# Kernel optimization log

Hardware: AMD Instinct MI355X
Metric: run time of the kernel (lower is better)

## Reference

```python
import jax, jax.numpy as jnp
import numpy as np

HID = 1024; HEADS = 16; HD = 64; INTER = 4096; NLAYERS = 4
PATCH = 16; IMG_SIZE = 1024; MAXSIDE = IMG_SIZE // PATCH
THETA = 10000.0; EPS = 1e-5; SCALE = HD ** -0.5


def setup_inputs() -> dict:
    key = jax.random.key(0)
    ks = jax.random.split(key, 11)
    s = 0.02
    w = lambda k, shape: jax.random.normal(k, shape, jnp.float32) * s
    return {
        "img0": jax.random.normal(ks[0], (3, 512, 512), jnp.float32),
        "img1": jax.random.normal(ks[1], (3, 512, 256), jnp.float32),
        "conv_w": w(ks[2], (HID, 3, PATCH, PATCH)),
        "ln_pre_w": jnp.ones((HID,), jnp.float32),
        "attn_norm_w": jnp.ones((NLAYERS, HID), jnp.float32),
        "q_w": w(ks[3], (NLAYERS, HID, HID)),
        "k_w": w(ks[4], (NLAYERS, HID, HID)),
        "v_w": w(ks[5], (NLAYERS, HID, HID)),
        "o_w": w(ks[6], (NLAYERS, HID, HID)),
        "ffn_norm_w": jnp.ones((NLAYERS, HID), jnp.float32),
        "gate_w": w(ks[7], (NLAYERS, INTER, HID)),
        "up_w": w(ks[8], (NLAYERS, INTER, HID)),
        "down_w": w(ks[9], (NLAYERS, HID, INTER)),
    }


def _rms(x, wt):
    return x * jax.lax.rsqrt(jnp.mean(x * x, axis=-1, keepdims=True) + EPS) * wt


def _rot_half(x):
    return jnp.concatenate([-x[..., HD // 2:], x[..., :HD // 2]], axis=-1)


def reference(img0, img1, conv_w, ln_pre_w, attn_norm_w, q_w, k_w, v_w, o_w,
              ffn_norm_w, gate_w, up_w, down_w):
    dn = ('NCHW', 'OIHW', 'NCHW')
    grids, embeds = [], []
    for img in (img0, img1):
        p = jax.lax.conv_general_dilated(img[None], conv_w, (PATCH, PATCH),
                                         'VALID', dimension_numbers=dn)  # [1,HID,h,w]
        h, wd = p.shape[2], p.shape[3]
        grids.append((h, wd))
        embeds.append(p.reshape(1, HID, h * wd).transpose(0, 2, 1))
    x = jnp.concatenate(embeds, axis=1)  # [1, S, HID]
    S = x.shape[1]
    x = _rms(x, ln_pre_w)

    # meshgrid position ids: h*MAXSIDE + w per image
    pids = jnp.concatenate([
        (jnp.arange(h)[:, None] * MAXSIDE + jnp.arange(wd)[None, :]).reshape(-1)
        for h, wd in grids])
    # Pixtral 2D RoPE frequency table
    freqs = 1.0 / THETA ** (jnp.arange(0, HD, 2, dtype=jnp.float32) / HD)  # [HD/2]
    fh = jnp.outer(jnp.arange(MAXSIDE, dtype=jnp.float32), freqs[::2])   # [64, HD/4]
    fw = jnp.outer(jnp.arange(MAXSIDE, dtype=jnp.float32), freqs[1::2])  # [64, HD/4]
    inv = jnp.concatenate([
        jnp.broadcast_to(fh[:, None, :], (MAXSIDE, MAXSIDE, HD // 4)),
        jnp.broadcast_to(fw[None, :, :], (MAXSIDE, MAXSIDE, HD // 4))],
        axis=-1).reshape(-1, HD // 2)
    inv = jnp.concatenate([inv, inv], axis=-1)  # [MAXSIDE^2, HD]
    emb = inv[pids]                              # [S, HD]
    cos = jnp.cos(emb)[None, None]               # [1,1,S,HD]
    sin = jnp.sin(emb)[None, None]

    # block-diagonal additive mask (images don't attend across each other)
    neg = jnp.finfo(jnp.float32).min
    mask = jnp.full((S, S), neg, jnp.float32)
    off = 0
    for h, wd in grids:
        n = h * wd
        mask = mask.at[off:off + n, off:off + n].set(0.0)
        off += n

    def layer(xc, p):
        an, qw, kw, vw, ow, fn, gw, uw, dw = p
        hn = _rms(xc, an)
        heads = lambda y, wm: jnp.einsum('bsd,ed->bse', y, wm).reshape(
            1, S, HEADS, HD).transpose(0, 2, 1, 3)  # [1,H,S,D]
        q, k, v = heads(hn, qw), heads(hn, kw), heads(hn, vw)
        q = q * cos + _rot_half(q) * sin
        k = k * cos + _rot_half(k) * sin
        scores = jnp.einsum('bhqd,bhkd->bhqk', q, k) * SCALE + mask
        aw = jax.nn.softmax(scores.astype(jnp.float32), axis=-1).astype(xc.dtype)
        o = jnp.einsum('bhqk,bhkd->bhqd', aw, v).transpose(0, 2, 1, 3).reshape(1, S, HID)
        h2 = xc + jnp.einsum('bsd,ed->bse', o, ow)
        m = _rms(h2, fn)
        ff = jnp.einsum(
            'bsi,di->bsd',
            jax.nn.silu(jnp.einsum('bsd,id->bsi', m, gw)) * jnp.einsum('bsd,id->bsi', m, uw),
            dw)
        return h2 + ff, None

    out, _ = jax.lax.scan(layer, x, (attn_norm_w, q_w, k_w, v_w, o_w,
                                     ffn_norm_w, gate_w, up_w, down_w))
    return out
```

## Files before the change

### kernel.cpp

```cpp
#include <hip/hip_runtime.h>
#include <hip/hip_bf16.h>
#include <math.h>

#define S_TOT 1536
#define S0    1024
#define HID   1024
#define HEADS 16
#define HD    64
#define INTER 4096
#define NLAYERS 4
#define KCONV 768
#define EPSV  1e-5f
#define SCALEV 0.125f
#define QKS   2048

typedef __attribute__((ext_vector_type(8))) __bf16 bf16x8;
typedef __attribute__((ext_vector_type(8))) unsigned short u16x8;
typedef __attribute__((ext_vector_type(4))) float f32x4;
typedef __attribute__((address_space(1))) void gvoid;
typedef __attribute__((address_space(3))) void lvoid;

__device__ __forceinline__ ushort f2bf(float f) {
    union { float f; unsigned u; } v; v.f = f;
    unsigned u = v.u;
    return (ushort)((u + 0x7FFFu + ((u >> 16) & 1u)) >> 16);
}
__device__ __forceinline__ float bf2f(ushort b) {
    union { unsigned u; float f; } v; v.u = ((unsigned)b) << 16;
    return v.f;
}

template<int N> __device__ __forceinline__ void wait_vm() {
    if constexpr (N == 0)      asm volatile("s_waitcnt vmcnt(0)" ::: "memory");
    else if constexpr (N == 2) asm volatile("s_waitcnt vmcnt(2)" ::: "memory");
    else if constexpr (N == 4) asm volatile("s_waitcnt vmcnt(4)" ::: "memory");
    else if constexpr (N == 8) asm volatile("s_waitcnt vmcnt(8)" ::: "memory");
    else                       asm volatile("s_waitcnt vmcnt(0)" ::: "memory");
}

__global__ __launch_bounds__(256) void cvt_kernel(
    const float* __restrict__ src, ushort* __restrict__ dst, int n4)
{
    int i = blockIdx.x * 256 + threadIdx.x;
    if (i < n4) {
        float4 v = ((const float4*)src)[i];
        ushort4 o;
        o.x = f2bf(v.x); o.y = f2bf(v.y); o.z = f2bf(v.z); o.w = f2bf(v.w);
        ((ushort4*)dst)[i] = o;
    }
}

__global__ __launch_bounds__(256) void cvt_layer_kernel(
    const float* __restrict__ qw, const float* __restrict__ kw,
    const float* __restrict__ vw, const float* __restrict__ ow,
    const float* __restrict__ gw, const float* __restrict__ uw,
    const float* __restrict__ dw, ushort* __restrict__ dst)
{
    int i = blockIdx.x * 256 + threadIdx.x;
    int e = i << 2;
    const float* src; int off; size_t de;
    if      (e < (1  << 20)) { src = qw; off = e;             de = e; }
    else if (e < (2  << 20)) { src = kw; off = e - (1 << 20); de = e; }
    else if (e < (3  << 20)) { src = vw; off = e - (2 << 20); de = e; }
    else if (e < (4  << 20)) { src = ow; off = e - (3 << 20); de = e; }
    else if (e < (8  << 20)) {
        src = gw; off = e - (4 << 20);
        int chan = off >> 10, col = off & 1023;
        de = (size_t)(4 << 20) + (size_t)(((chan >> 4) << 5) + (chan & 15)) * 1024 + col;
    }
    else if (e < (12 << 20)) {
        src = uw; off = e - (8 << 20);
        int chan = off >> 10, col = off & 1023;
        de = (size_t)(4 << 20) + (size_t)(((chan >> 4) << 5) + 16 + (chan & 15)) * 1024 + col;
    }
    else                     { src = dw; off = e - (12 << 20); de = e; }
    float4 v = *(const float4*)(src + off);
    ushort4 o;
    o.x = f2bf(v.x); o.y = f2bf(v.y); o.z = f2bf(v.z); o.w = f2bf(v.w);
    *(ushort4*)(dst + de) = o;
}

__global__ __launch_bounds__(256) void im2col_kernel(
    const float* __restrict__ img0, const float* __restrict__ img1,
    ushort* __restrict__ P)
{
    int s = blockIdx.x;
    const float* img; int W, ph, pw;
    if (s < S0) { img = img0; W = 512; ph = s >> 5; pw = s & 31; }
    else { int t = s - S0; img = img1; W = 256; ph = t >> 4; pw = t & 15; }
    for (int k = threadIdx.x; k < KCONV; k += 256) {
        int c = k >> 8; int r = k & 255; int y = r >> 4; int x = r & 15;
        P[(size_t)s * KCONV + k] =
            f2bf(img[(size_t)c * 512 * W + (size_t)(ph * 16 + y) * W + (pw * 16 + x)]);
    }
}

#define GEMM2P_CORE(BM_, BN_, NLA_, NLB_)                                        \
    auto stage = [&](int b, int k0) {                                            \
        _Pragma("unroll")                                                        \
        for (int i_ = 0; i_ < NLA_; ++i_) {                                      \
            int idx = t + i_ * 256;                                              \
            int r_ = idx >> 2, c8_ = (idx & 3) << 3;                             \
            __builtin_amdgcn_global_load_lds(                                    \
                (gvoid*)(A + (size_t)(bm + r_) * K + k0 + c8_),                  \
                (lvoid*)(&As[b][idx * 8]), 16, 0, 0);                            \
        }                                                                        \
        _Pragma("unroll")                                                        \
        for (int i_ = 0; i_ < NLB_; ++i_) {                                      \
            int idx = t + i_ * 256;                                              \
            int r_ = idx >> 2, c8_ = (idx & 3) << 3;                             \
            __builtin_amdgcn_global_load_lds(                                    \
                (gvoid*)(B + (size_t)(bn + r_) * K + k0 + c8_),                  \
                (lvoid*)(&Bs[b][idx * 8]), 16, 0, 0);                            \
        }                                                                        \
    };

template<int BM, int BN, bool OUT_BF16>
__global__ __launch_bounds__(256) void gemm2p(
    const ushort* __restrict__ A, const ushort* __restrict__ B,
    void* __restrict__ Cout, int M, int N, int K)
{
    constexpr int WMT = BM / 32, WNT = BN / 32;
    constexpr int NLA = (BM * 32) / (8 * 256);
    constexpr int NLB = (BN * 32) / (8 * 256);
    constexpr int NL  = NLA + NLB;
    __shared__ ushort As[2][BM * 32];
    __shared__ ushort Bs[2][BN * 32];
    const int t = threadIdx.x;
    const int bm = blockIdx.x * BM, bn = blockIdx.y * BN;
    const int wave = t >> 6, lane = t & 63;
    const int wm = (wave & 1) * (BM / 2), wn = (wave >> 1) * (BN / 2);
    const int frow = lane & 15, fq = lane >> 4;
    GEMM2P_CORE(BM, BN, NLA, NLB)

    f32x4 acc[WMT][WNT];
    #pragma unroll
    for (int i = 0; i < WMT; ++i)
        #pragma unroll
        for (int j = 0; j < WNT; ++j) acc[i][j] = (f32x4){0.f, 0.f, 0.f, 0.f};

    stage(0, 0);
    int cur = 0;
    for (int k0 = 0; k0 < K; k0 += 32) {
        const bool more = (k0 + 32) < K;
        if (more) { stage(cur ^ 1, k0 + 32); wait_vm<NL>(); }
        else      { wait_vm<0>(); }
        __builtin_amdgcn_s_barrier();
        __builtin_amdgcn_sched_barrier(0);
        bf16x8 af[WMT], bfr[WNT];
        #pragma unroll
        for (int i = 0; i < WMT; ++i)
            af[i] = *(const bf16x8*)(&As[cur][(wm + 16 * i + frow) * 32 + fq * 8]);
        #pragma unroll
        for (int j = 0; j < WNT; ++j)
            bfr[j] = *(const bf16x8*)(&Bs[cur][(wn + 16 * j + frow) * 32 + fq * 8]);
        asm volatile("s_waitcnt lgkmcnt(0)" ::: "memory");
        __builtin_amdgcn_sched_barrier(0);
        __builtin_amdgcn_s_barrier();
        #pragma unroll
        for (int i = 0; i < WMT; ++i)
            #pragma unroll
            for (int j = 0; j < WNT; ++j)
                acc[i][j] = __builtin_amdgcn_mfma_f32_16x16x32_bf16(
                    af[i], bfr[j], acc[i][j], 0, 0, 0);
        cur ^= 1;
    }
    #pragma unroll
    for (int i = 0; i < WMT; ++i) {
        #pragma unroll
        for (int j = 0; j < WNT; ++j) {
            #pragma unroll
            for (int r = 0; r < 4; ++r) {
                int row = bm + wm + 16 * i + fq * 4 + r;
                int col = bn + wn + 16 * j + frow;
                float vv = acc[i][j][r];
                if (OUT_BF16) ((ushort*)Cout)[(size_t)row * N + col] = f2bf(vv);
                else          ((float*)Cout)[(size_t)row * N + col] = vv;
            }
        }
    }
}

__global__ __launch_bounds__(256) void gemm2p_qkv(
    const ushort* __restrict__ A, const ushort* __restrict__ B,
    ushort* __restrict__ qkb, ushort* __restrict__ vb,
    const float* __restrict__ cs, const float* __restrict__ sn, int K)
{
    constexpr int BM = 128, BN = 128;
    __shared__ ushort As[2][BM * 32];
    __shared__ ushort Bs[2][BN * 32];
    const int t = threadIdx.x;
    const int bm = blockIdx.x * BM, bn = blockIdx.y * BN;
    const int wave = t >> 6, lane = t & 63;
    const int wm = (wave & 1) * 64, wn = (wave >> 1) * 64;
    const int frow = lane & 15, fq = lane >> 4;
    GEMM2P_CORE(BM, BN, 2, 2)

    f32x4 acc[4][4];
    #pragma unroll
    for (int i = 0; i < 4; ++i)
        #pragma unroll
        for (int j = 0; j < 4; ++j) acc[i][j] = (f32x4){0.f, 0.f, 0.f, 0.f};

    stage(0, 0);
    int cur = 0;
    for (int k0 = 0; k0 < K; k0 += 32) {
        const bool more = (k0 + 32) < K;
        if (more) { stage(cur ^ 1, k0 + 32); wait_vm<4>(); }
        else      { wait_vm<0>(); }
        __builtin_amdgcn_s_barrier();
        __builtin_amdgcn_sched_barrier(0);
        bf16x8 af[4], bfr[4];
        #pragma unroll
        for (int i = 0; i < 4; ++i)
            af[i] = *(const bf16x8*)(&As[cur][(wm + 16 * i + frow) * 32 + fq * 8]);
        #pragma unroll
        for (int j = 0; j < 4; ++j)
            bfr[j] = *(const bf16x8*)(&Bs[cur][(wn + 16 * j + frow) * 32 + fq * 8]);
        asm volatile("s_waitcnt lgkmcnt(0)" ::: "memory");
        __builtin_amdgcn_sched_barrier(0);
        __builtin_amdgcn_s_barrier();
        #pragma unroll
        for (int i = 0; i < 4; ++i)
            #pragma unroll
            for (int j = 0; j < 4; ++j)
                acc[i][j] = __builtin_amdgcn_mfma_f32_16x16x32_bf16(
                    af[i], bfr[j], acc[i][j], 0, 0, 0);
        cur ^= 1;
    }
    const int colbase = bn + wn;
    const int part = colbase >> 10;
    if (part < 2) {
        #pragma unroll
        for (int i = 0; i < 4; ++i) {
            #pragma unroll
            for (int r = 0; r < 4; ++r) {
                int row = bm + wm + 16 * i + fq * 4 + r;
                float cv0 = cs[row * 32 + frow],      sv0 = sn[row * 32 + frow];
                float cv1 = cs[row * 32 + 16 + frow], sv1 = sn[row * 32 + 16 + frow];
                float xa0 = acc[i][0][r], xa1 = acc[i][1][r];
                float xb0 = acc[i][2][r], xb1 = acc[i][3][r];
                ushort* dst = qkb + (size_t)row * QKS + (part << 10) + (colbase & 1023) + frow;
                dst[0]  = f2bf(xa0 * cv0 - xb0 * sv0);
                dst[16] = f2bf(xa1 * cv1 - xb1 * sv1);
                dst[32] = f2bf(xb0 * cv0 + xa0 * sv0);
                dst[48] = f2bf(xb1 * cv1 + xa1 * sv1);
            }
        }
    } else {
        #pragma unroll
        for (int i = 0; i < 4; ++i)
            #pragma unroll
            for (int j = 0; j < 4; ++j)
                #pragma unroll
                for (int r = 0; r < 4; ++r) {
                    int row = bm + wm + 16 * i + fq * 4 + r;
                    vb[(size_t)row * 1024 + (colbase & 1023) + 16 * j + frow] =
                        f2bf(acc[i][j][r]);
                }
    }
}

__global__ __launch_bounds__(256) void gemm2p_gu(
    const ushort* __restrict__ A, const ushort* __restrict__ B,
    ushort* __restrict__ gb, int K)
{
    constexpr int BM = 128, BN = 128;
    __shared__ ushort As[2][BM * 32];
    __shared__ ushort Bs[2][BN * 32];
    const int t = threadIdx.x;
    const int bm = blockIdx.x * BM, bn = blockIdx.y * BN;
    const int wave = t >> 6, lane = t & 63;
    const int wm = (wave & 1) * 64, wn = (wave >> 1) * 64;
    const int frow = lane & 15, fq = lane >> 4;
    GEMM2P_CORE(BM, BN, 2, 2)

    f32x4 acc[4][4];
    #pragma unroll
    for (int i = 0; i < 4; ++i)
        #pragma unroll
        for (int j = 0; j < 4; ++j) acc[i][j] = (f32x4){0.f, 0.f, 0.f, 0.f};

    stage(0, 0);
    int cur = 0;
    for (int k0 = 0; k0 < K; k0 += 32) {
        const bool more = (k0 + 32) < K;
        if (more) { stage(cur ^ 1, k0 + 32); wait_vm<4>(); }
        else      { wait_vm<0>(); }
        __builtin_amdgcn_s_barrier();
        __builtin_amdgcn_sched_barrier(0);
        bf16x8 af[4], bfr[4];
        #pragma unroll
        for (int i = 0; i < 4; ++i)
            af[i] = *(const bf16x8*)(&As[cur][(wm + 16 * i + frow) * 32 + fq * 8]);
        #pragma unroll
        for (int j = 0; j < 4; ++j)
            bfr[j] = *(const bf16x8*)(&Bs[cur][(wn + 16 * j + frow) * 32 + fq * 8]);
        asm volatile("s_waitcnt lgkmcnt(0)" ::: "memory");
        __builtin_amdgcn_sched_barrier(0);
        __builtin_amdgcn_s_barrier();
        #pragma unroll
        for (int i = 0; i < 4; ++i)
            #pragma unroll
            for (int j = 0; j < 4; ++j)
                acc[i][j] = __builtin_amdgcn_mfma_f32_16x16x32_bf16(
                    af[i], bfr[j], acc[i][j], 0, 0, 0);
        cur ^= 1;
    }
    #pragma unroll
    for (int i = 0; i < 4; ++i) {
        #pragma unroll
        for (int jp = 0; jp < 2; ++jp) {
            int chan = ((bn + wn) >> 1) + jp * 16 + frow;
            #pragma unroll
            for (int r = 0; r < 4; ++r) {
                int row = bm + wm + 16 * i + fq * 4 + r;
                float g = acc[i][2 * jp][r], u = acc[i][2 * jp + 1][r];
                float sg = 1.f / (1.f + __expf(-g));
                gb[(size_t)row * INTER + chan] = f2bf(g * sg * u);
            }
        }
    }
}

template<int SPLITK>
__global__ __launch_bounds__(256) void gemm2p_sk(
    const ushort* __restrict__ A, const ushort* __restrict__ B,
    float* __restrict__ P, int M, int N, int K)
{
    constexpr int BM = 128, BN = 128;
    __shared__ ushort As[2][BM * 32];
    __shared__ ushort Bs[2][BN * 32];
    const int t = threadIdx.x;
    const int bm = blockIdx.x * BM, bn = blockIdx.y * BN;
    const int kc = K / SPLITK;
    const int kb = blockIdx.z * kc, ke = kb + kc;
    const int wave = t >> 6, lane = t & 63;
    const int wm = (wave & 1) * 64, wn = (wave >> 1) * 64;
    const int frow = lane & 15, fq = lane >> 4;
    GEMM2P_CORE(BM, BN, 2, 2)

    f32x4 acc[4][4];
    #pragma unroll
    for (int i = 0; i < 4; ++i)
        #pragma unroll
        for (int j = 0; j < 4; ++j) acc[i][j] = (f32x4){0.f, 0.f, 0.f, 0.f};

    stage(0, kb);
    int cur = 0;
    for (int k0 = kb; k0 < ke; k0 += 32) {
        const bool more = (k0 + 32) < ke;
        if (more) { stage(cur ^ 1, k0 + 32); wait_vm<4>(); }
        else      { wait_vm<0>(); }
        __builtin_amdgcn_s_barrier();
        __builtin_amdgcn_sched_barrier(0);
        bf16x8 af[4], bfr[4];
        #pragma unroll
        for (int i = 0; i < 4; ++i)
            af[i] = *(const bf16x8*)(&As[cur][(wm + 16 * i + frow) * 32 + fq * 8]);
        #pragma unroll
        for (int j = 0; j < 4; ++j)
            bfr[j] = *(const bf16x8*)(&Bs[cur][(wn + 16 * j + frow) * 32 + fq * 8]);
        asm volatile("s_waitcnt lgkmcnt(0)" ::: "memory");
        __builtin_amdgcn_sched_barrier(0);
        __builtin_amdgcn_s_barrier();
        #pragma unroll
        for (int i = 0; i < 4; ++i)
            #pragma unroll
            for (int j = 0; j < 4; ++j)
                acc[i][j] = __builtin_amdgcn_mfma_f32_16x16x32_bf16(
                    af[i], bfr[j], acc[i][j], 0, 0, 0);
        cur ^= 1;
    }
    float* Pz = P + (size_t)blockIdx.z * M * N;
    #pragma unroll
    for (int i = 0; i < 4; ++i) {
        #pragma unroll
        for (int j = 0; j < 4; ++j) {
            #pragma unroll
            for (int r = 0; r < 4; ++r) {
                int row = bm + wm + 16 * i + fq * 4 + r;
                int col = bn + wn + 16 * j + frow;
                Pz[(size_t)row * N + col] = acc[i][j][r];
            }
        }
    }
}

__global__ __launch_bounds__(256) void reduce4_kernel(
    const float* __restrict__ P, float* __restrict__ x, int n4)
{
    int i = blockIdx.x * 256 + threadIdx.x;
    if (i >= n4) return;
    const int n = n4 << 2;
    float4 a  = ((const float4*)x)[i];
    float4 p0 = ((const float4*)P)[i];
    float4 p1 = ((const float4*)(P + (size_t)n))[i];
    float4 p2 = ((const float4*)(P + (size_t)2 * n))[i];
    float4 p3 = ((const float4*)(P + (size_t)3 * n))[i];
    a.x += p0.x + p1.x + p2.x + p3.x;
    a.y += p0.y + p1.y + p2.y + p3.y;
    a.z += p0.z + p1.z + p2.z + p3.z;
    a.w += p0.w + p1.w + p2.w + p3.w;
    ((float4*)x)[i] = a;
}

__global__ __launch_bounds__(256) void rms_kernel(
    const float* __restrict__ in, const float* __restrict__ w,
    float* __restrict__ out)
{
    int row = blockIdx.x;
    const float* xr = in + (size_t)row * HID;
    float ss = 0.f;
    for (int i = threadIdx.x; i < HID; i += 256) { float v = xr[i]; ss += v * v; }
    #pragma unroll
    for (int off = 32; off > 0; off >>= 1) ss += __shfl_down(ss, off, 64);
    __shared__ float red[4];
    int wid = threadIdx.x >> 6;
    if ((threadIdx.x & 63) == 0) red[wid] = ss;
    __syncthreads();
    if (threadIdx.x == 0)
        red[0] = rsqrtf((red[0] + red[1] + red[2] + red[3]) / HID + EPSV);
    __syncthreads();
    float rs = red[0];
    for (int i = threadIdx.x; i < HID; i += 256)
        out[(size_t)row * HID + i] = xr[i] * rs * w[i];
}

__global__ __launch_bounds__(256) void rms_bf_kernel(
    const float* __restrict__ in, const float* __restrict__ w,
    ushort* __restrict__ out)
{
    int row = blockIdx.x;
    const float* xr = in + (size_t)row * HID;
    float ss = 0.f;
    for (int i = threadIdx.x; i < HID; i += 256) { float v = xr[i]; ss += v * v; }
    #pragma unroll
    for (int off = 32; off > 0; off >>= 1) ss += __shfl_down(ss, off, 64);
    __shared__ float red[4];
    int wid = threadIdx.x >> 6;
    if ((threadIdx.x & 63) == 0) red[wid] = ss;
    __syncthreads();
    if (threadIdx.x == 0)
        red[0] = rsqrtf((red[0] + red[1] + red[2] + red[3]) / HID + EPSV);
    __syncthreads();
    float rs = red[0];
    for (int i = threadIdx.x; i < HID; i += 256)
        out[(size_t)row * HID + i] = f2bf(xr[i] * rs * w[i]);
}

__global__ void rope_tab_kernel(float* __restrict__ cs, float* __restrict__ sn)
{
    int s = blockIdx.x; int j = threadIdx.x;
    int h, w;
    if (s < S0) { h = s >> 5; w = s & 31; }
    else { int t = s - S0; h = t >> 4; w = t & 15; }
    float f;
    if (j < 16) f = (float)h * powf(10000.f, -(4.f * j) / 64.f);
    else        f = (float)w * powf(10000.f, -(4.f * (j - 16) + 2.f) / 64.f);
    cs[s * 32 + j] = cosf(f);
    sn[s * 32 + j] = sinf(f);
}

__global__ __launch_bounds__(256) void vtrans_bf_kernel(
    const ushort* __restrict__ vb, ushort* __restrict__ vT)
{
    __shared__ ushort T[64][72];
    int st = blockIdx.x;
    int hh = blockIdx.y;
    int s0 = st << 6;
    int t = threadIdx.x;
    #pragma unroll
    for (int i = 0; i < 2; ++i) {
        int u = t + (i << 8);
        int r = u >> 3, c8 = (u & 7) << 3;
        u16x8 v = *(const u16x8*)(vb + (size_t)(s0 + r) * 1024 + hh * HD + c8);
        *(u16x8*)(&T[r][c8]) = v;
    }
    __syncthreads();
    int d = t >> 2, sg = (t & 3) << 4;
    ushort buf[16];
    #pragma unroll
    for (int j = 0; j < 16; ++j) buf[j] = T[sg + j][d];
    ushort* dst = vT + ((size_t)hh * HD + d) * S_TOT + s0 + sg;
    *(u16x8*)dst = *(u16x8*)buf;
    *(u16x8*)(dst + 8) = *(u16x8*)(buf + 8);
}

__global__ __launch_bounds__(256) void flash_mfma_kernel(
    const ushort* __restrict__ qkb, const ushort* __restrict__ vT,
    ushort* __restrict__ o)
{
    __shared__ ushort Ks[64 * 72];
    __shared__ ushort Vt[64 * 72];
    __shared__ ushort Ps[4 * 16 * 72];
    int tile = blockIdx.x;
    int hh = blockIdx.y;
    int segStart, q0, nkt;
    if (tile < 16) { segStart = 0; q0 = tile << 6; nkt = 16; }
    else { segStart = S0; q0 = S0 + ((tile - 16) << 6); nkt = 8; }
    const int t = threadIdx.x;
    const int wave = t >> 6, lane = t & 63;
    const int c = lane & 15, fq = lane >> 4;
    const int wq = wave << 4;
    ushort* Pw = Ps + wave * 16 * 72;

    bf16x8 qf[2];
    #pragma unroll
    for (int ks = 0; ks < 2; ++ks)
        qf[ks] = *(const bf16x8*)(qkb + (size_t)(q0 + wq + c) * QKS + hh * HD + ks * 32 + fq * 8);

    float m_i[4], l_i[4];
    f32x4 accO[4];
    #pragma unroll
    for (int r = 0; r < 4; ++r) { m_i[r] = -1e30f; l_i[r] = 0.f; }
    #pragma unroll
    for (int nt = 0; nt < 4; ++nt) accO[nt] = (f32x4){0.f, 0.f, 0.f, 0.f};

    for (int kt = 0; kt < nkt; ++kt) {
        int kbase = segStart + (kt << 6);
        __syncthreads();
        #pragma unroll
        for (int i = 0; i < 2; ++i) {
            int u = t + (i << 8);
            int r = u >> 3, c8 = (u & 7) << 3;
            u16x8 kv = *(const u16x8*)(qkb + (size_t)(kbase + r) * QKS + 1024 + hh * HD + c8);
            *(u16x8*)(Ks + r * 72 + c8) = kv;
            u16x8 vv = *(const u16x8*)(vT + ((size_t)hh * HD + r) * S_TOT + kbase + c8);
            *(u16x8*)(Vt + r * 72 + c8) = vv;
        }
        __syncthreads();

        f32x4 acc[4];
        #pragma unroll
        for (int nt = 0; nt < 4; ++nt) acc[nt] = (f32x4){0.f, 0.f, 0.f, 0.f};
        #pragma unroll
        for (int ks = 0; ks < 2; ++ks) {
            #pragma unroll
            for (int nt = 0; nt < 4; ++nt) {
                bf16x8 bfr = *(const bf16x8*)(Ks + (nt * 16 + c) * 72 + ks * 32 + fq * 8);
                acc[nt] = __builtin_amdgcn_mfma_f32_16x16x32_bf16(qf[ks], bfr, acc[nt], 0, 0, 0);
            }
        }

        #pragma unroll
        for (int r = 0; r < 4; ++r) {
            float s0v = acc[0][r] * SCALEV, s1v = acc[1][r] * SCALEV;
            float s2v = acc[2][r] * SCALEV, s3v = acc[3][r] * SCALEV;
            float rm = fmaxf(fmaxf(s0v, s1v), fmaxf(s2v, s3v));
            #pragma unroll
            for (int msk = 1; msk < 16; msk <<= 1)
                rm = fmaxf(rm, __shfl_xor(rm, msk, 64));
            float mn = fmaxf(m_i[r], rm);
            float al = __expf(m_i[r] - mn);
            float p0 = __expf(s0v - mn), p1 = __expf(s1v - mn);
            float p2 = __expf(s2v - mn), p3 = __expf(s3v - mn);
            float rs = p0 + p1 + p2 + p3;
            #pragma unroll
            for (int msk = 1; msk < 16; msk <<= 1)
                rs += __shfl_xor(rs, msk, 64);
            l_i[r] = l_i[r] * al + rs;
            m_i[r] = mn;
            #pragma unroll
            for (int nt = 0; nt < 4; ++nt) accO[nt][r] *= al;
            int qrow = (fq << 2) + r;
            Pw[qrow * 72 + 0  + c] = f2bf(p0);
            Pw[qrow * 72 + 16 + c] = f2bf(p1);
            Pw[qrow * 72 + 32 + c] = f2bf(p2);
            Pw[qrow * 72 + 48 + c] = f2bf(p3);
        }

        #pragma unroll
        for (int ks = 0; ks < 2; ++ks) {
            bf16x8 pa = *(const bf16x8*)(Pw + c * 72 + ks * 32 + fq * 8);
            #pragma unroll
            for (int nt = 0; nt < 4; ++nt) {
                bf16x8 bv = *(const bf16x8*)(Vt + (nt * 16 + c) * 72 + ks * 32 + fq * 8);
                accO[nt] = __builtin_amdgcn_mfma_f32_16x16x32_bf16(pa, bv, accO[nt], 0, 0, 0);
            }
        }
    }

    #pragma unroll
    for (int r = 0; r < 4; ++r) {
        float inv = 1.f / l_i[r];
        int row = q0 + wq + (fq << 2) + r;
        #pragma unroll
        for (int nt = 0; nt < 4; ++nt)
            o[(size_t)row * HID + hh * HD + nt * 16 + c] = f2bf(accO[nt][r] * inv);
    }
}

__global__ __launch_bounds__(256) void copy_kernel(
    const float* __restrict__ src, float* __restrict__ dst, int n)
{
    int i = blockIdx.x * 256 + threadIdx.x;
    if (i < n) dst[i] = src[i];
}

extern "C" void kernel_launch(void* const* d_in, const int* in_sizes, int n_in,
                              void* d_out, int out_size, void* d_ws, size_t ws_size,
                              hipStream_t stream)
{
    const float* img0        = (const float*)d_in[0];
    const float* img1        = (const float*)d_in[1];
    const float* conv_w      = (const float*)d_in[2];
    const float* ln_pre_w    = (const float*)d_in[3];
    const float* attn_norm_w = (const float*)d_in[4];
    const float* q_w         = (const float*)d_in[5];
    const float* k_w         = (const float*)d_in[6];
    const float* v_w         = (const float*)d_in[7];
    const float* o_w         = (const float*)d_in[8];
    const float* ffn_norm_w  = (const float*)d_in[9];
    const float* gate_w      = (const float*)d_in[10];
    const float* up_w        = (const float*)d_in[11];
    const float* down_w      = (const float*)d_in[12];

    char* p = (char*)d_ws;
    float* x    = (float*)p;   p += (size_t)1572864 * 4;
    float* cs   = (float*)p;   p += (size_t)49152 * 4;
    float* sn   = (float*)p;   p += (size_t)49152 * 4;
    ushort* qkb = (ushort*)p;  p += (size_t)3145728 * 2;
    ushort* vb  = (ushort*)p;  p += (size_t)1572864 * 2;
    ushort* vTb = (ushort*)p;  p += (size_t)1572864 * 2;
    ushort* hnb = (ushort*)p;  p += (size_t)1572864 * 2;
    ushort* obb = (ushort*)p;  p += (size_t)1572864 * 2;
    ushort* gb  = (ushort*)p;  p += (size_t)6291456 * 2;
    float* skP  = (float*)p;   p += (size_t)6291456 * 4;
    ushort* Pb  = (ushort*)p;  p += (size_t)1179648 * 2;
    ushort* cvb = (ushort*)p;  p += (size_t)786432 * 2;
    ushort* wbuf= (ushort*)p;  p += (size_t)16777216 * 2;

    ushort* wqkv = wbuf;
    ushort* wo   = wbuf + 3145728;
    ushort* wgu  = wbuf + 4194304;
    ushort* wdn  = wbuf + 12582912;

    dim3 blk(256);

    cvt_kernel<<<768, blk, 0, stream>>>(conv_w, cvb, 786432 / 4);
    im2col_kernel<<<S_TOT, blk, 0, stream>>>(img0, img1, Pb);
    gemm2p<64, 64, false><<<dim3(24, 16), blk, 0, stream>>>(
        Pb, cvb, x, S_TOT, HID, KCONV);
    rms_kernel<<<S_TOT, blk, 0, stream>>>(x, ln_pre_w, x);
    rope_tab_kernel<<<S_TOT, 32, 0, stream>>>(cs, sn);

    for (int l = 0; l < NLAYERS; ++l) {
        cvt_layer_kernel<<<16384, blk, 0, stream>>>(
            q_w + (size_t)l * 1048576, k_w + (size_t)l * 1048576,
            v_w + (size_t)l * 1048576, o_w + (size_t)l * 1048576,
            gate_w + (size_t)l * 4194304, up_w + (size_t)l * 4194304,
            down_w + (size_t)l * 4194304, wbuf);

        rms_bf_kernel<<<S_TOT, blk, 0, stream>>>(x, attn_norm_w + (size_t)l * HID, hnb);
        gemm2p_qkv<<<dim3(12, 24), blk, 0, stream>>>(
            hnb, wqkv, qkb, vb, cs, sn, HID);
        vtrans_bf_kernel<<<dim3(24, HEADS), blk, 0, stream>>>(vb, vTb);
        flash_mfma_kernel<<<dim3(24, HEADS), blk, 0, stream>>>(qkb, vTb, obb);
        gemm2p_sk<4><<<dim3(12, 8, 4), blk, 0, stream>>>(
            obb, wo, skP, S_TOT, HID, HID);
        reduce4_kernel<<<1536, blk, 0, stream>>>(skP, x, S_TOT * HID / 4);
        rms_bf_kernel<<<S_TOT, blk, 0, stream>>>(x, ffn_norm_w + (size_t)l * HID, hnb);
        gemm2p_gu<<<dim3(12, 64), blk, 0, stream>>>(hnb, wgu, gb, HID);
        gemm2p_sk<4><<<dim3(12, 8, 4), blk, 0, stream>>>(
            gb, wdn, skP, S_TOT, HID, INTER);
        reduce4_kernel<<<1536, blk, 0, stream>>>(skP, x, S_TOT * HID / 4);
    }
    copy_kernel<<<(S_TOT * HID) / 256, blk, 0, stream>>>(x, (float*)d_out, S_TOT * HID);
}
```

Baseline: 927.9 us.

## Triple-buffer GEMM loads, fuse V transpose into QKV epilogue, fuse reduce+RMS

All GEMM kernels move from a double-buffered to a triple-buffered LDS pipeline with a single barrier per k-step, and raise wave priority around the MFMA block. The QKV GEMM epilogue now writes V directly in transposed per-head layout, which removes the separate transpose kernel and its buffer. The split-K reduction after the O projection is fused with the following RMS norm into one kernel, saving a launch and a pass over x. Extra LDS per block may lower occupancy, and the transposed V stores are strided 8-byte writes.

```diff
diff --git a/kernel.cpp b/kernel.cpp
--- a/kernel.cpp
+++ b/kernel.cpp
@@ -95,7 +95,7 @@
     }
 }
 
-#define GEMM2P_CORE(BM_, BN_, NLA_, NLB_)                                        \
+#define STAGE_LAMBDA(NLA_, NLB_)                                                 \
     auto stage = [&](int b, int k0) {                                            \
         _Pragma("unroll")                                                        \
         for (int i_ = 0; i_ < NLA_; ++i_) {                                      \
@@ -115,8 +115,25 @@
         }                                                                        \
     };
 
+#define LOOP3B_HEAD(NL_, KBASE_)                                                 \
+    stage(0, KBASE_); stage(1, KBASE_ + 32);                                     \
+    int cbuf = 0, sbuf = 2;                                                      \
+    for (int kt = 0; kt < NKT; ++kt) {                                           \
+        if (kt + 1 < NKT) wait_vm<NL_>(); else wait_vm<0>();                     \
+        __builtin_amdgcn_sched_barrier(0);                                       \
+        __builtin_amdgcn_s_barrier();                                            \
+        __builtin_amdgcn_sched_barrier(0);                                       \
+        if (kt + 2 < NKT) {                                                      \
+            stage(sbuf, KBASE_ + ((kt + 2) << 5));                               \
+            sbuf = (sbuf == 2) ? 0 : sbuf + 1;                                   \
+        }
+
+#define LOOP3B_TAIL                                                              \
+        cbuf = (cbuf == 2) ? 0 : cbuf + 1;                                       \
+    }
+
 template<int BM, int BN, bool OUT_BF16>
-__global__ __launch_bounds__(256) void gemm2p(
+__global__ __launch_bounds__(256) void gemm3b(
     const ushort* __restrict__ A, const ushort* __restrict__ B,
     void* __restrict__ Cout, int M, int N, int K)
 {
@@ -124,14 +141,14 @@
     constexpr int NLA = (BM * 32) / (8 * 256);
     constexpr int NLB = (BN * 32) / (8 * 256);
     constexpr int NL  = NLA + NLB;
-    __shared__ ushort As[2][BM * 32];
-    __shared__ ushort Bs[2][BN * 32];
+    __shared__ ushort As[3][BM * 32];
+    __shared__ ushort Bs[3][BN * 32];
     const int t = threadIdx.x;
     const int bm = blockIdx.x * BM, bn = blockIdx.y * BN;
     const int wave = t >> 6, lane = t & 63;
     const int wm = (wave & 1) * (BM / 2), wn = (wave >> 1) * (BN / 2);
     const int frow = lane & 15, fq = lane >> 4;
-    GEMM2P_CORE(BM, BN, NLA, NLB)
+    STAGE_LAMBDA(NLA, NLB)
 
     f32x4 acc[WMT][WNT];
     #pragma unroll
@@ -139,32 +156,24 @@
         #pragma unroll
         for (int j = 0; j < WNT; ++j) acc[i][j] = (f32x4){0.f, 0.f, 0.f, 0.f};
 
-    stage(0, 0);
-    int cur = 0;
-    for (int k0 = 0; k0 < K; k0 += 32) {
-        const bool more = (k0 + 32) < K;
-        if (more) { stage(cur ^ 1, k0 + 32); wait_vm<NL>(); }
-        else      { wait_vm<0>(); }
-        __builtin_amdgcn_s_barrier();
-        __builtin_amdgcn_sched_barrier(0);
+    const int NKT = K >> 5;
+    LOOP3B_HEAD(NL, 0)
         bf16x8 af[WMT], bfr[WNT];
         #pragma unroll
         for (int i = 0; i < WMT; ++i)
-            af[i] = *(const bf16x8*)(&As[cur][(wm + 16 * i + frow) * 32 + fq * 8]);
+            af[i] = *(const bf16x8*)(&As[cbuf][(wm + 16 * i + frow) * 32 + fq * 8]);
         #pragma unroll
         for (int j = 0; j < WNT; ++j)
-            bfr[j] = *(const bf16x8*)(&Bs[cur][(wn + 16 * j + frow) * 32 + fq * 8]);
-        asm volatile("s_waitcnt lgkmcnt(0)" ::: "memory");
-        __builtin_amdgcn_sched_barrier(0);
-        __builtin_amdgcn_s_barrier();
+            bfr[j] = *(const bf16x8*)(&Bs[cbuf][(wn + 16 * j + frow) * 32 + fq * 8]);
+        __builtin_amdgcn_s_setprio(1);
         #pragma unroll
         for (int i = 0; i < WMT; ++i)
             #pragma unroll
             for (int j = 0; j < WNT; ++j)
                 acc[i][j] = __builtin_amdgcn_mfma_f32_16x16x32_bf16(
                     af[i], bfr[j], acc[i][j], 0, 0, 0);
-        cur ^= 1;
-    }
+        __builtin_amdgcn_s_setprio(0);
+    LOOP3B_TAIL
     #pragma unroll
     for (int i = 0; i < WMT; ++i) {
         #pragma unroll
@@ -181,20 +190,20 @@
     }
 }
 
-__global__ __launch_bounds__(256) void gemm2p_qkv(
+__global__ __launch_bounds__(256) void gemm3b_qkv(
     const ushort* __restrict__ A, const ushort* __restrict__ B,
-    ushort* __restrict__ qkb, ushort* __restrict__ vb,
+    ushort* __restrict__ qkb, ushort* __restrict__ vT,
     const float* __restrict__ cs, const float* __restrict__ sn, int K)
 {
     constexpr int BM = 128, BN = 128;
-    __shared__ ushort As[2][BM * 32];
-    __shared__ ushort Bs[2][BN * 32];
+    __shared__ ushort As[3][BM * 32];
+    __shared__ ushort Bs[3][BN * 32];
     const int t = threadIdx.x;
     const int bm = blockIdx.x * BM, bn = blockIdx.y * BN;
     const int wave = t >> 6, lane = t & 63;
     const int wm = (wave & 1) * 64, wn = (wave >> 1) * 64;
     const int frow = lane & 15, fq = lane >> 4;
-    GEMM2P_CORE(BM, BN, 2, 2)
+    STAGE_LAMBDA(2, 2)
 
     f32x4 acc[4][4];
     #pragma unroll
@@ -202,32 +211,24 @@
         #pragma unroll
         for (int j = 0; j < 4; ++j) acc[i][j] = (f32x4){0.f, 0.f, 0.f, 0.f};
 
-    stage(0, 0);
-    int cur = 0;
-    for (int k0 = 0; k0 < K; k0 += 32) {
-        const bool more = (k0 + 32) < K;
-        if (more) { stage(cur ^ 1, k0 + 32); wait_vm<4>(); }
-        else      { wait_vm<0>(); }
-        __builtin_amdgcn_s_barrier();
-        __builtin_amdgcn_sched_barrier(0);
+    const int NKT = K >> 5;
+    LOOP3B_HEAD(4, 0)
         bf16x8 af[4], bfr[4];
         #pragma unroll
         for (int i = 0; i < 4; ++i)
-            af[i] = *(const bf16x8*)(&As[cur][(wm + 16 * i + frow) * 32 + fq * 8]);
+            af[i] = *(const bf16x8*)(&As[cbuf][(wm + 16 * i + frow) * 32 + fq * 8]);
         #pragma unroll
         for (int j = 0; j < 4; ++j)
-            bfr[j] = *(const bf16x8*)(&Bs[cur][(wn + 16 * j + frow) * 32 + fq * 8]);
-        asm volatile("s_waitcnt lgkmcnt(0)" ::: "memory");
-        __builtin_amdgcn_sched_barrier(0);
-        __builtin_amdgcn_s_barrier();
+            bfr[j] = *(const bf16x8*)(&Bs[cbuf][(wn + 16 * j + frow) * 32 + fq * 8]);
+        __builtin_amdgcn_s_setprio(1);
         #pragma unroll
         for (int i = 0; i < 4; ++i)
             #pragma unroll
             for (int j = 0; j < 4; ++j)
                 acc[i][j] = __builtin_amdgcn_mfma_f32_16x16x32_bf16(
                     af[i], bfr[j], acc[i][j], 0, 0, 0);
-        cur ^= 1;
-    }
+        __builtin_amdgcn_s_setprio(0);
+    LOOP3B_TAIL
     const int colbase = bn + wn;
     const int part = colbase >> 10;
     if (part < 2) {
@@ -248,32 +249,35 @@
             }
         }
     } else {
-        #pragma unroll
-        for (int i = 0; i < 4; ++i)
-            #pragma unroll
-            for (int j = 0; j < 4; ++j)
-                #pragma unroll
-                for (int r = 0; r < 4; ++r) {
-                    int row = bm + wm + 16 * i + fq * 4 + r;
-                    vb[(size_t)row * 1024 + (colbase & 1023) + 16 * j + frow] =
-                        f2bf(acc[i][j][r]);
-                }
-    }
-}
-
-__global__ __launch_bounds__(256) void gemm2p_gu(
+        const int hh = (colbase - 2048) >> 6;
+        #pragma unroll
+        for (int i = 0; i < 4; ++i) {
+            int row = bm + wm + 16 * i + (fq << 2);
+            #pragma unroll
+            for (int j = 0; j < 4; ++j) {
+                int d = 16 * j + frow;
+                ushort4 o4;
+                o4.x = f2bf(acc[i][j][0]); o4.y = f2bf(acc[i][j][1]);
+                o4.z = f2bf(acc[i][j][2]); o4.w = f2bf(acc[i][j][3]);
+                *(ushort4*)(vT + ((size_t)hh * HD + d) * S_TOT + row) = o4;
+            }
+        }
+    }
+}
+
+__global__ __launch_bounds__(256) void gemm3b_gu(
     const ushort* __restrict__ A, const ushort* __restrict__ B,
     ushort* __restrict__ gb, int K)
 {
     constexpr int BM = 128, BN = 128;
-    __shared__ ushort As[2][BM * 32];
-    __shared__ ushort Bs[2][BN * 32];
+    __shared__ ushort As[3][BM * 32];
+    __shared__ ushort Bs[3][BN * 32];
     const int t = threadIdx.x;
     const int bm = blockIdx.x * BM, bn = blockIdx.y * BN;
     const int wave = t >> 6, lane = t & 63;
     const int wm = (wave & 1) * 64, wn = (wave >> 1) * 64;
     const int frow = lane & 15, fq = lane >> 4;
-    GEMM2P_CORE(BM, BN, 2, 2)
+    STAGE_LAMBDA(2, 2)
 
     f32x4 acc[4][4];
     #pragma unroll
@@ -281,41 +285,33 @@
         #pragma unroll
         for (int j = 0; j < 4; ++j) acc[i][j] = (f32x4){0.f, 0.f, 0.f, 0.f};
 
-    stage(0, 0);
-    int cur = 0;
-    for (int k0 = 0; k0 < K; k0 += 32) {
-        const bool more = (k0 + 32) < K;
-        if (more) { stage(cur ^ 1, k0 + 32); wait_vm<4>(); }
-        else      { wait_vm<0>(); }
-        __builtin_amdgcn_s_barrier();
-        __builtin_amdgcn_sched_barrier(0);
+    const int NKT = K >> 5;
+    LOOP3B_HEAD(4, 0)
         bf16x8 af[4], bfr[4];
         #pragma unroll
         for (int i = 0; i < 4; ++i)
-            af[i] = *(const bf16x8*)(&As[cur][(wm + 16 * i + frow) * 32 + fq * 8]);
+            af[i] = *(const bf16x8*)(&As[cbuf][(wm + 16 * i + frow) * 32 + fq * 8]);
         #pragma unroll
         for (int j = 0; j < 4; ++j)
-            bfr[j] = *(const bf16x8*)(&Bs[cur][(wn + 16 * j + frow) * 32 + fq * 8]);
-        asm volatile("s_waitcnt lgkmcnt(0)" ::: "memory");
-        __builtin_amdgcn_sched_barrier(0);
-        __builtin_amdgcn_s_barrier();
+            bfr[j] = *(const bf16x8*)(&Bs[cbuf][(wn + 16 * j + frow) * 32 + fq * 8]);
+        __builtin_amdgcn_s_setprio(1);
         #pragma unroll
         for (int i = 0; i < 4; ++i)
             #pragma unroll
             for (int j = 0; j < 4; ++j)
                 acc[i][j] = __builtin_amdgcn_mfma_f32_16x16x32_bf16(
                     af[i], bfr[j], acc[i][j], 0, 0, 0);
-        cur ^= 1;
-    }
+        __builtin_amdgcn_s_setprio(0);
+    LOOP3B_TAIL
     #pragma unroll
     for (int i = 0; i < 4; ++i) {
         #pragma unroll
-        for (int jp = 0; jp < 2; ++jp) {
-            int chan = ((bn + wn) >> 1) + jp * 16 + frow;
+        for (int p = 0; p < 2; ++p) {
+            int chan = ((bn + wn) >> 1) + p * 16 + frow;
             #pragma unroll
             for (int r = 0; r < 4; ++r) {
                 int row = bm + wm + 16 * i + fq * 4 + r;
-                float g = acc[i][2 * jp][r], u = acc[i][2 * jp + 1][r];
+                float g = acc[i][2 * p][r], u = acc[i][2 * p + 1][r];
                 float sg = 1.f / (1.f + __expf(-g));
                 gb[(size_t)row * INTER + chan] = f2bf(g * sg * u);
             }
@@ -324,21 +320,21 @@
 }
 
 template<int SPLITK>
-__global__ __launch_bounds__(256) void gemm2p_sk(
+__global__ __launch_bounds__(256) void gemm3b_sk(
     const ushort* __restrict__ A, const ushort* __restrict__ B,
     float* __restrict__ P, int M, int N, int K)
 {
     constexpr int BM = 128, BN = 128;
-    __shared__ ushort As[2][BM * 32];
-    __shared__ ushort Bs[2][BN * 32];
+    __shared__ ushort As[3][BM * 32];
+    __shared__ ushort Bs[3][BN * 32];
     const int t = threadIdx.x;
     const int bm = blockIdx.x * BM, bn = blockIdx.y * BN;
     const int kc = K / SPLITK;
-    const int kb = blockIdx.z * kc, ke = kb + kc;
+    const int kb = blockIdx.z * kc;
     const int wave = t >> 6, lane = t & 63;
     const int wm = (wave & 1) * 64, wn = (wave >> 1) * 64;
     const int frow = lane & 15, fq = lane >> 4;
-    GEMM2P_CORE(BM, BN, 2, 2)
+    STAGE_LAMBDA(2, 2)
 
     f32x4 acc[4][4];
     #pragma unroll
@@ -346,32 +342,24 @@
         #pragma unroll
         for (int j = 0; j < 4; ++j) acc[i][j] = (f32x4){0.f, 0.f, 0.f, 0.f};
 
-    stage(0, kb);
-    int cur = 0;
-    for (int k0 = kb; k0 < ke; k0 += 32) {
-        const bool more = (k0 + 32) < ke;
-        if (more) { stage(cur ^ 1, k0 + 32); wait_vm<4>(); }
-        else      { wait_vm<0>(); }
-        __builtin_amdgcn_s_barrier();
-        __builtin_amdgcn_sched_barrier(0);
+    const int NKT = kc >> 5;
+    LOOP3B_HEAD(4, kb)
         bf16x8 af[4], bfr[4];
         #pragma unroll
         for (int i = 0; i < 4; ++i)
-            af[i] = *(const bf16x8*)(&As[cur][(wm + 16 * i + frow) * 32 + fq * 8]);
+            af[i] = *(const bf16x8*)(&As[cbuf][(wm + 16 * i + frow) * 32 + fq * 8]);
         #pragma unroll
         for (int j = 0; j < 4; ++j)
-            bfr[j] = *(const bf16x8*)(&Bs[cur][(wn + 16 * j + frow) * 32 + fq * 8]);
-        asm volatile("s_waitcnt lgkmcnt(0)" ::: "memory");
-        __builtin_amdgcn_sched_barrier(0);
-        __builtin_amdgcn_s_barrier();
+            bfr[j] = *(const bf16x8*)(&Bs[cbuf][(wn + 16 * j + frow) * 32 + fq * 8]);
+        __builtin_amdgcn_s_setprio(1);
         #pragma unroll
         for (int i = 0; i < 4; ++i)
             #pragma unroll
             for (int j = 0; j < 4; ++j)
                 acc[i][j] = __builtin_amdgcn_mfma_f32_16x16x32_bf16(
                     af[i], bfr[j], acc[i][j], 0, 0, 0);
-        cur ^= 1;
-    }
+        __builtin_amdgcn_s_setprio(0);
+    LOOP3B_TAIL
     float* Pz = P + (size_t)blockIdx.z * M * N;
     #pragma unroll
     for (int i = 0; i < 4; ++i) {
@@ -405,6 +393,37 @@
     ((float4*)x)[i] = a;
 }
 
+__global__ __launch_bounds__(256) void reduce_rms_bf_kernel(
+    const float* __restrict__ P, float* __restrict__ x,
+    const float* __restrict__ w, ushort* __restrict__ out)
+{
+    int row = blockIdx.x, t = threadIdx.x;
+    size_t off = (size_t)row * HID + t * 4;
+    float4 a = *(const float4*)(x + off);
+    #pragma unroll
+    for (int z = 0; z < 4; ++z) {
+        float4 p = *(const float4*)(P + (size_t)z * S_TOT * HID + off);
+        a.x += p.x; a.y += p.y; a.z += p.z; a.w += p.w;
+    }
+    *(float4*)(x + off) = a;
+    float ss = a.x * a.x + a.y * a.y + a.z * a.z + a.w * a.w;
+    #pragma unroll
+    for (int o = 32; o > 0; o >>= 1) ss += __shfl_down(ss, o, 64);
+    __shared__ float red[4];
+    int wid = t >> 6;
+    if ((t & 63) == 0) red[wid] = ss;
+    __syncthreads();
+    if (t == 0)
+        red[0] = rsqrtf((red[0] + red[1] + red[2] + red[3]) / HID + EPSV);
+    __syncthreads();
+    float rs = red[0];
+    const float* wp = w + t * 4;
+    ushort4 o4;
+    o4.x = f2bf(a.x * rs * wp[0]); o4.y = f2bf(a.y * rs * wp[1]);
+    o4.z = f2bf(a.z * rs * wp[2]); o4.w = f2bf(a.w * rs * wp[3]);
+    *(ushort4*)(out + off) = o4;
+}
+
 __global__ __launch_bounds__(256) void rms_kernel(
     const float* __restrict__ in, const float* __restrict__ w,
     float* __restrict__ out)
@@ -460,31 +479,6 @@
     else        f = (float)w * powf(10000.f, -(4.f * (j - 16) + 2.f) / 64.f);
     cs[s * 32 + j] = cosf(f);
     sn[s * 32 + j] = sinf(f);
-}
-
-__global__ __launch_bounds__(256) void vtrans_bf_kernel(
-    const ushort* __restrict__ vb, ushort* __restrict__ vT)
-{
-    __shared__ ushort T[64][72];
-    int st = blockIdx.x;
-    int hh = blockIdx.y;
-    int s0 = st << 6;
-    int t = threadIdx.x;
-    #pragma unroll
-    for (int i = 0; i < 2; ++i) {
-        int u = t + (i << 8);
-        int r = u >> 3, c8 = (u & 7) << 3;
-        u16x8 v = *(const u16x8*)(vb + (size_t)(s0 + r) * 1024 + hh * HD + c8);
-        *(u16x8*)(&T[r][c8]) = v;
-    }
-    __syncthreads();
-    int d = t >> 2, sg = (t & 3) << 4;
-    ushort buf[16];
-    #pragma unroll
-    for (int j = 0; j < 16; ++j) buf[j] = T[sg + j][d];
-    ushort* dst = vT + ((size_t)hh * HD + d) * S_TOT + s0 + sg;
-    *(u16x8*)dst = *(u16x8*)buf;
-    *(u16x8*)(dst + 8) = *(u16x8*)(buf + 8);
 }
 
 __global__ __launch_bounds__(256) void flash_mfma_kernel(
@@ -621,7 +615,6 @@
     float* cs   = (float*)p;   p += (size_t)49152 * 4;
     float* sn   = (float*)p;   p += (size_t)49152 * 4;
     ushort* qkb = (ushort*)p;  p += (size_t)3145728 * 2;
-    ushort* vb  = (ushort*)p;  p += (size_t)1572864 * 2;
     ushort* vTb = (ushort*)p;  p += (size_t)1572864 * 2;
     ushort* hnb = (ushort*)p;  p += (size_t)1572864 * 2;
     ushort* obb = (ushort*)p;  p += (size_t)1572864 * 2;
@@ -640,7 +633,7 @@
 
     cvt_kernel<<<768, blk, 0, stream>>>(conv_w, cvb, 786432 / 4);
     im2col_kernel<<<S_TOT, blk, 0, stream>>>(img0, img1, Pb);
-    gemm2p<64, 64, false><<<dim3(24, 16), blk, 0, stream>>>(
+    gemm3b<64, 64, false><<<dim3(24, 16), blk, 0, stream>>>(
         Pb, cvb, x, S_TOT, HID, KCONV);
     rms_kernel<<<S_TOT, blk, 0, stream>>>(x, ln_pre_w, x);
     rope_tab_kernel<<<S_TOT, 32, 0, stream>>>(cs, sn);
@@ -653,16 +646,15 @@
             down_w + (size_t)l * 4194304, wbuf);
 
         rms_bf_kernel<<<S_TOT, blk, 0, stream>>>(x, attn_norm_w + (size_t)l * HID, hnb);
-        gemm2p_qkv<<<dim3(12, 24), blk, 0, stream>>>(
-            hnb, wqkv, qkb, vb, cs, sn, HID);
-        vtrans_bf_kernel<<<dim3(24, HEADS), blk, 0, stream>>>(vb, vTb);
+        gemm3b_qkv<<<dim3(12, 24), blk, 0, stream>>>(
+            hnb, wqkv, qkb, vTb, cs, sn, HID);
         flash_mfma_kernel<<<dim3(24, HEADS), blk, 0, stream>>>(qkb, vTb, obb);
-        gemm2p_sk<4><<<dim3(12, 8, 4), blk, 0, stream>>>(
+        gemm3b_sk<4><<<dim3(12, 8, 4), blk, 0, stream>>>(
             obb, wo, skP, S_TOT, HID, HID);
-        reduce4_kernel<<<1536, blk, 0, stream>>>(skP, x, S_TOT * HID / 4);
-        rms_bf_kernel<<<S_TOT, blk, 0, stream>>>(x, ffn_norm_w + (size_t)l * HID, hnb);
-        gemm2p_gu<<<dim3(12, 64), blk, 0, stream>>>(hnb, wgu, gb, HID);
-        gemm2p_sk<4><<<dim3(12, 8, 4), blk, 0, stream>>>(
+        reduce_rms_bf_kernel<<<S_TOT, blk, 0, stream>>>(
+            skP, x, ffn_norm_w + (size_t)l * HID, hnb);
+        gemm3b_gu<<<dim3(12, 64), blk, 0, stream>>>(hnb, wgu, gb, HID);
+        gemm3b_sk<4><<<dim3(12, 8, 4), blk, 0, stream>>>(
             gb, wdn, skP, S_TOT, HID, INTER);
         reduce4_kernel<<<1536, blk, 0, stream>>>(skP, x, S_TOT * HID / 4);
     }
```

After: 918.8 us. No clear change (-1.0%).
